# Performance work log

Hardware: AMD Instinct MI355X
Metric: run time of the kernel (lower is better)

Reference implementation:

```python
import jax, jax.numpy as jnp
import numpy as np

DEGREE = 8


def setup_inputs() -> dict:
    key = jax.random.key(0)
    k1, k2 = jax.random.split(key)
    x = jax.random.normal(k1, (8192, 1024), dtype=jnp.float32)
    # xavier_normal-ish scale for coeffs [input_dim, output_dim, degree+1]
    std = (2.0 / (1024 + 1024)) ** 0.5
    cheby_coeffs = jax.random.normal(k2, (1024, 1024, DEGREE + 1), dtype=jnp.float32) * std
    return {"x": x, "cheby_coeffs": cheby_coeffs}


def _cheby(x, degree):
    # x: [B, I] in [-1, 1]; returns T: [B, I, degree+1]
    T = [jnp.ones_like(x), x]
    for n in range(2, degree + 1):
        T.append(2.0 * x * T[-1] - T[-2])
    return jnp.stack(T, axis=-1)


def reference(x, cheby_coeffs) -> jnp.ndarray:
    input_dim = cheby_coeffs.shape[0]
    degree = cheby_coeffs.shape[-1] - 1
    x = x.reshape(-1, input_dim)
    xmin = jnp.min(x, axis=1, keepdims=True)
    xmax = jnp.max(x, axis=1, keepdims=True)
    x = 2.0 * (x - xmin) / (xmax - xmin) - 1.0
    T = _cheby(x, degree)  # [B, I, D+1]
    y = jnp.einsum('bij,ioj->bo', T, cheby_coeffs)
    return y
```

## Files before the change

### kernel.cpp

```cpp
#include <hip/hip_runtime.h>
#include <hip/hip_bf16.h>


typedef __attribute__((ext_vector_type(8))) short bf16x8s;
typedef __attribute__((ext_vector_type(4))) float f32x4;

constexpr int BROWS = 8192;
constexpr int IDIM  = 1024;
constexpr int ODIM  = 1024;
constexpr int DEG1  = 9;
constexpr int KP    = 8;
constexpr int KD    = IDIM * KP;
constexpr int KH    = KD / 2;

__device__ __forceinline__ ushort f2bf(float f) {
  return ((__hip_bfloat16_raw)__float2bfloat16(f)).x;
}

__device__ __forceinline__ void gload_lds16(const void* g, void* l) {
  __builtin_amdgcn_global_load_lds(
      (const __attribute__((address_space(1))) unsigned int*)g,
      (__attribute__((address_space(3))) unsigned int*)l, 16, 0, 0);
}

__global__ __launch_bounds__(256) void zero_bias_kernel(float* __restrict__ bias) {
  bias[blockIdx.x * 256 + threadIdx.x] = 0.0f;
}

__global__ __launch_bounds__(256) void build_a_kernel(const float* __restrict__ x,
                                                      ushort* __restrict__ A2) {
  __shared__ float red[8];
  const int b = blockIdx.x, t = threadIdx.x, lane = t & 63, wv = t >> 6;
  const float* xr = x + (size_t)b * IDIM;
  const float4 v = ((const float4*)xr)[t];
  float mn = fminf(fminf(v.x, v.y), fminf(v.z, v.w));
  float mx = fmaxf(fmaxf(v.x, v.y), fmaxf(v.z, v.w));
#pragma unroll
  for (int off = 32; off >= 1; off >>= 1) {
    mn = fminf(mn, __shfl_xor(mn, off));
    mx = fmaxf(mx, __shfl_xor(mx, off));
  }
  if (lane == 0) { red[wv] = mn; red[4 + wv] = mx; }
  __syncthreads();
  mn = fminf(fminf(red[0], red[1]), fminf(red[2], red[3]));
  mx = fmaxf(fmaxf(red[4], red[5]), fmaxf(red[6], red[7]));
  const float sc = 2.0f / (mx - mn);
  const float of = -mn * sc - 1.0f;

  uint4* adst = (uint4*)(A2 + (size_t)b * KD);
#pragma unroll
  for (int c = 0; c < 4; ++c) {
    const int i = c * 256 + t;
    const float xn = fmaf(sc, xr[i], of);
    const float T2 = 2.f * xn * xn - 1.f;
    const float T3 = 2.f * xn * T2 - xn;
    const float T4 = 2.f * xn * T3 - T2;
    const float T5 = 2.f * xn * T4 - T3;
    const float T6 = 2.f * xn * T5 - T4;
    const float T7 = 2.f * xn * T6 - T5;
    const float T8 = 2.f * xn * T7 - T6;
    uint4 w;
    w.x = (uint)f2bf(xn) | ((uint)f2bf(T2) << 16);
    w.y = (uint)f2bf(T3) | ((uint)f2bf(T4) << 16);
    w.z = (uint)f2bf(T5) | ((uint)f2bf(T6) << 16);
    w.w = (uint)f2bf(T7) | ((uint)f2bf(T8) << 16);
    adst[i] = w;
  }
}

__global__ __launch_bounds__(256) void build_b_kernel(const float* __restrict__ coeffs,
                                                      ushort* __restrict__ B2T,
                                                      float* __restrict__ bias) {
  __shared__ __align__(16) ushort tile[64 * 256];
  __shared__ float lb[64];
  const int i0 = blockIdx.x * 32;
  const int o0 = blockIdx.y * 64;
  const int t  = threadIdx.x;
  if (t < 64) lb[t] = 0.0f;
  __syncthreads();
  for (int idx = t; idx < 18432; idx += 256) {
    const int i_l = idx / 576;
    const int rem = idx - i_l * 576;
    const float v = coeffs[((size_t)(i0 + i_l) * ODIM + o0) * DEG1 + rem];
    const int o_l = rem / 9;
    const int j   = rem - o_l * 9;
    if (j == 0) atomicAdd(&lb[o_l], v);
    else tile[o_l * 256 + i_l * KP + (j - 1)] = f2bf(v);
  }
  __syncthreads();
  for (int idx = t; idx < 2048; idx += 256) {
    const int o_l = idx >> 5;
    const int w   = idx & 31;
    uint4* gdst = (uint4*)(B2T + (size_t)(o0 + o_l) * KD + i0 * KP);
    gdst[w] = ((const uint4*)tile)[idx];
  }
  if (t < 64) atomicAdd(&bias[o0 + t], lb[t]);
}

__global__ __launch_bounds__(512, 4) void gemm_kernel(const ushort* __restrict__ A2,
                                                      const ushort* __restrict__ B2T,
                                                      const float* __restrict__ bias,
                                                      float* __restrict__ out) {
  constexpr int BK = 64;
  __shared__ __align__(16) ushort Sm[32768];
  const int t    = threadIdx.x;
  const int wave = t >> 6;
  const int lane = t & 63;
  const int g    = wave >> 2;
  const int w4   = wave & 3;
  const int wr   = w4 >> 1;
  const int wc   = w4 & 1;
  const int c16  = lane & 15;
  const int quad = lane >> 4;
  const int rowBase = blockIdx.y * 128;
  const int colBase = blockIdx.x * 128;

  ushort* As = Sm + g * 8192;
  ushort* Bs = Sm + 16384 + g * 8192;

  const int tp   = t & 255;
  const int srow = tp >> 3;
  const int scol = (tp & 7) ^ (srow & 7);
  const ushort* aB = A2  + (size_t)(rowBase + srow) * KD + (size_t)g * KH + scol * 8;
  const ushort* bB = B2T + (size_t)(colBase + srow) * KD + (size_t)g * KH + scol * 8;
  ushort* lA = As + tp * 8;
  ushort* lB = Bs + tp * 8;

  f32x4 acc[4][4];
#pragma unroll
  for (int a = 0; a < 4; ++a)
#pragma unroll
    for (int b = 0; b < 4; ++b) acc[a][b] = (f32x4){0.f, 0.f, 0.f, 0.f};

  for (int ip = 0; ip < KH / BK; ++ip) {
    const size_t ko = (size_t)ip * BK;
    __syncthreads();
#pragma unroll
    for (int rr = 0; rr < 4; ++rr) {
      gload_lds16(aB + (size_t)rr * 32 * KD + ko, lA + rr * 2048);
      gload_lds16(bB + (size_t)rr * 32 * KD + ko, lB + rr * 2048);
    }
    __syncthreads();

#pragma unroll
    for (int kh = 0; kh < 2; ++kh) {
      const int cx = ((kh * 4 + quad) ^ (c16 & 7)) * 8;
      bf16x8s afr[4], bfr[4];
#pragma unroll
      for (int tm = 0; tm < 4; ++tm)
        afr[tm] = *(const bf16x8s*)&As[(wr * 64 + tm * 16 + c16) * BK + cx];
#pragma unroll
      for (int tn = 0; tn < 4; ++tn)
        bfr[tn] = *(const bf16x8s*)&Bs[(wc * 64 + tn * 16 + c16) * BK + cx];
#pragma unroll
      for (int tm = 0; tm < 4; ++tm)
#pragma unroll
        for (int tn = 0; tn < 4; ++tn)
          acc[tm][tn] = __builtin_amdgcn_mfma_f32_16x16x32_bf16(afr[tm], bfr[tn],
                                                                acc[tm][tn], 0, 0, 0);
    }
  }

  __syncthreads();
  float* Ct = (float*)Sm;
  if (g == 1) {
#pragma unroll
    for (int tm = 0; tm < 4; ++tm)
#pragma unroll
      for (int tn = 0; tn < 4; ++tn) {
        const int lr0 = wr * 64 + tm * 16 + quad * 4;
        const int cl  = wc * 64 + tn * 16 + c16;
#pragma unroll
        for (int r = 0; r < 4; ++r) Ct[(lr0 + r) * 128 + cl] = acc[tm][tn][r];
      }
  }
  __syncthreads();
  if (g == 0) {
#pragma unroll
    for (int tm = 0; tm < 4; ++tm)
#pragma unroll
      for (int tn = 0; tn < 4; ++tn) {
        const int lr0 = wr * 64 + tm * 16 + quad * 4;
        const int cl  = wc * 64 + tn * 16 + c16;
        const float bv = bias[colBase + cl];
#pragma unroll
        for (int r = 0; r < 4; ++r)
          out[(size_t)(rowBase + lr0 + r) * ODIM + colBase + cl] =
              acc[tm][tn][r] + Ct[(lr0 + r) * 128 + cl] + bv;
      }
  }
}

extern "C" void kernel_launch(void* const* d_in, const int* in_sizes, int n_in,
                              void* d_out, int out_size, void* d_ws, size_t ws_size,
                              hipStream_t stream) {
  const float* x      = (const float*)d_in[0];
  const float* coeffs = (const float*)d_in[1];
  float* out = (float*)d_out;

  char* ws = (char*)d_ws;
  float*  bias = (float*)ws;
  ushort* B2T  = (ushort*)(ws + 65536);
  ushort* A2   = (ushort*)(ws + 65536 + (size_t)ODIM * KD * 2);

  zero_bias_kernel<<<ODIM / 256, 256, 0, stream>>>(bias);
  build_a_kernel<<<BROWS, 256, 0, stream>>>(x, A2);
  build_b_kernel<<<dim3(IDIM / 32, ODIM / 64), 256, 0, stream>>>(coeffs, B2T, bias);
  gemm_kernel<<<dim3(ODIM / 128, BROWS / 128), 512, 0, stream>>>(A2, B2T, bias, out);
}
```

Measured before the change: 314.6 us.

## Restructure GEMM into triple-buffered 256x128 tiles with prefetch and block swizzle

The GEMM drops the split-K design, where two wave groups each covered half of K and were reduced through shared memory. Each block now computes a 256x128 tile over the full K using eight waves. Global-to-LDS loads are triple-buffered and issued two iterations ahead, with explicit vmcnt waits, raw barriers and setprio around the MFMA bursts. A block-index swizzle improves L2 reuse. This aims to hide load latency behind MFMA work and drop the split-K reduction, at the cost of more LDS per block and lower occupancy.

```diff
diff --git a/kernel.cpp b/kernel.cpp
--- a/kernel.cpp
+++ b/kernel.cpp
@@ -11,7 +11,6 @@
 constexpr int DEG1  = 9;
 constexpr int KP    = 8;
 constexpr int KD    = IDIM * KP;
-constexpr int KH    = KD / 2;
 
 __device__ __forceinline__ ushort f2bf(float f) {
   return ((__hip_bfloat16_raw)__float2bfloat16(f)).x;
@@ -97,97 +96,116 @@
   if (t < 64) atomicAdd(&bias[o0 + t], lb[t]);
 }
 
-__global__ __launch_bounds__(512, 4) void gemm_kernel(const ushort* __restrict__ A2,
+#define GEMM_PHASE(CX, ISSUE_STMT, TAILWAIT_STMT)                                 \
+  {                                                                               \
+    bf16x8s afr[4], bfr[4];                                                       \
+    _Pragma("unroll")                                                             \
+    for (int m = 0; m < 4; ++m)                                                   \
+      afr[m] = *(const bf16x8s*)&Asb[aoff + m * (16 * 64) + (CX)];                \
+    _Pragma("unroll")                                                             \
+    for (int n = 0; n < 4; ++n)                                                   \
+      bfr[n] = *(const bf16x8s*)&Bsb[boff + n * (16 * 64) + (CX)];                \
+    ISSUE_STMT;                                                                   \
+    __builtin_amdgcn_s_barrier();                                                 \
+    asm volatile("s_waitcnt lgkmcnt(0)" ::: "memory");                            \
+    __builtin_amdgcn_s_setprio(1);                                                \
+    _Pragma("unroll")                                                             \
+    for (int m = 0; m < 4; ++m)                                                   \
+      _Pragma("unroll")                                                           \
+      for (int n = 0; n < 4; ++n)                                                 \
+        acc[m][n] = __builtin_amdgcn_mfma_f32_16x16x32_bf16(afr[m], bfr[n],       \
+                                                            acc[m][n], 0, 0, 0);  \
+    __builtin_amdgcn_s_setprio(0);                                                \
+    TAILWAIT_STMT;                                                                \
+    __builtin_amdgcn_s_barrier();                                                 \
+  }
+
+__global__ __launch_bounds__(512, 2) void gemm_kernel(const ushort* __restrict__ A2,
                                                       const ushort* __restrict__ B2T,
                                                       const float* __restrict__ bias,
                                                       float* __restrict__ out) {
-  constexpr int BK = 64;
-  __shared__ __align__(16) ushort Sm[32768];
+  constexpr int BK    = 64;
+  constexpr int KT    = KD / BK;
+  constexpr int ABUF  = 256 * BK;
+  constexpr int BBUF  = 128 * BK;
+  constexpr int BUFSZ = ABUF + BBUF;
+  __shared__ __align__(16) ushort Sm[3 * BUFSZ];
+
   const int t    = threadIdx.x;
+  const int lane = t & 63;
   const int wave = t >> 6;
-  const int lane = t & 63;
-  const int g    = wave >> 2;
-  const int w4   = wave & 3;
-  const int wr   = w4 >> 1;
-  const int wc   = w4 & 1;
+  const int wr   = wave >> 1;
+  const int wc   = wave & 1;
   const int c16  = lane & 15;
   const int quad = lane >> 4;
-  const int rowBase = blockIdx.y * 128;
-  const int colBase = blockIdx.x * 128;
-
-  ushort* As = Sm + g * 8192;
-  ushort* Bs = Sm + 16384 + g * 8192;
-
-  const int tp   = t & 255;
-  const int srow = tp >> 3;
-  const int scol = (tp & 7) ^ (srow & 7);
-  const ushort* aB = A2  + (size_t)(rowBase + srow) * KD + (size_t)g * KH + scol * 8;
-  const ushort* bB = B2T + (size_t)(colBase + srow) * KD + (size_t)g * KH + scol * 8;
-  ushort* lA = As + tp * 8;
-  ushort* lB = Bs + tp * 8;
+
+  const int orig = blockIdx.y * 8 + blockIdx.x;
+  const int swz  = (orig & 7) * 32 + (orig >> 3);
+  const int rowBase = (swz >> 3) * 256;
+  const int colBase = (swz & 7) * 128;
+
+  const int trow = t >> 3;
+  const int scol = (t & 7) ^ (trow & 7);
+  const ushort* aB = A2  + (size_t)(rowBase + trow) * KD + scol * 8;
+  const ushort* bB = B2T + (size_t)(colBase + trow) * KD + scol * 8;
+  ushort* uA = Sm + t * 8;
+  ushort* uB = Sm + ABUF + t * 8;
+
+  auto issA = [&](int buf, size_t ko, int a) {
+    gload_lds16(aB + (size_t)a * (64 * KD) + ko, uA + buf * BUFSZ + a * 4096);
+  };
+  auto issB = [&](int buf, size_t ko, int b2) {
+    gload_lds16(bB + (size_t)b2 * (64 * KD) + ko, uB + buf * BUFSZ + b2 * 4096);
+  };
+
+  const int aoff = (wr * 64 + c16) * BK;
+  const int boff = (wc * 64 + c16) * BK;
+  const int cx0  = ((0 + quad) ^ (c16 & 7)) * 8;
+  const int cx1  = ((4 + quad) ^ (c16 & 7)) * 8;
 
   f32x4 acc[4][4];
 #pragma unroll
-  for (int a = 0; a < 4; ++a)
-#pragma unroll
-    for (int b = 0; b < 4; ++b) acc[a][b] = (f32x4){0.f, 0.f, 0.f, 0.f};
-
-  for (int ip = 0; ip < KH / BK; ++ip) {
-    const size_t ko = (size_t)ip * BK;
-    __syncthreads();
-#pragma unroll
-    for (int rr = 0; rr < 4; ++rr) {
-      gload_lds16(aB + (size_t)rr * 32 * KD + ko, lA + rr * 2048);
-      gload_lds16(bB + (size_t)rr * 32 * KD + ko, lB + rr * 2048);
+  for (int m = 0; m < 4; ++m)
+#pragma unroll
+    for (int n = 0; n < 4; ++n) acc[m][n] = (f32x4){0.f, 0.f, 0.f, 0.f};
+
+  issA(0, 0, 0); issA(0, 0, 1); issA(0, 0, 2); issA(0, 0, 3);
+  issB(0, 0, 0); issB(0, 0, 1);
+  issA(1, BK, 0); issA(1, BK, 1); issA(1, BK, 2); issA(1, BK, 3);
+  issB(1, BK, 0); issB(1, BK, 1);
+  asm volatile("s_waitcnt vmcnt(6)" ::: "memory");
+  __builtin_amdgcn_s_barrier();
+
+  int cur = 0;
+  for (int it = 0; it < KT; ++it) {
+    const ushort* Asb = Sm + cur * BUFSZ;
+    const ushort* Bsb = Asb + ABUF;
+    const int nb = (cur >= 1) ? cur - 1 : 2;
+    const size_t ko = (size_t)(it + 2) * BK;
+    const bool pf = (it < KT - 2);
+
+    GEMM_PHASE(cx0,
+      if (pf) { issA(nb, ko, 0); issA(nb, ko, 1); issA(nb, ko, 2); },
+      ;);
+    GEMM_PHASE(cx1,
+      if (pf) { issA(nb, ko, 3); issB(nb, ko, 0); issB(nb, ko, 1); },
+      if (pf)              { asm volatile("s_waitcnt vmcnt(6)" ::: "memory"); }
+      else if (it == KT-2) { asm volatile("s_waitcnt vmcnt(0)" ::: "memory"); });
+
+    cur = (cur == 2) ? 0 : cur + 1;
+  }
+
+#pragma unroll
+  for (int n = 0; n < 4; ++n) {
+    const int col = colBase + wc * 64 + n * 16 + c16;
+    const float bv = bias[col];
+#pragma unroll
+    for (int m = 0; m < 4; ++m) {
+      const int r0 = rowBase + wr * 64 + m * 16 + quad * 4;
+#pragma unroll
+      for (int r = 0; r < 4; ++r)
+        out[(size_t)(r0 + r) * ODIM + col] = acc[m][n][r] + bv;
     }
-    __syncthreads();
-
-#pragma unroll
-    for (int kh = 0; kh < 2; ++kh) {
-      const int cx = ((kh * 4 + quad) ^ (c16 & 7)) * 8;
-      bf16x8s afr[4], bfr[4];
-#pragma unroll
-      for (int tm = 0; tm < 4; ++tm)
-        afr[tm] = *(const bf16x8s*)&As[(wr * 64 + tm * 16 + c16) * BK + cx];
-#pragma unroll
-      for (int tn = 0; tn < 4; ++tn)
-        bfr[tn] = *(const bf16x8s*)&Bs[(wc * 64 + tn * 16 + c16) * BK + cx];
-#pragma unroll
-      for (int tm = 0; tm < 4; ++tm)
-#pragma unroll
-        for (int tn = 0; tn < 4; ++tn)
-          acc[tm][tn] = __builtin_amdgcn_mfma_f32_16x16x32_bf16(afr[tm], bfr[tn],
-                                                                acc[tm][tn], 0, 0, 0);
-    }
-  }
-
-  __syncthreads();
-  float* Ct = (float*)Sm;
-  if (g == 1) {
-#pragma unroll
-    for (int tm = 0; tm < 4; ++tm)
-#pragma unroll
-      for (int tn = 0; tn < 4; ++tn) {
-        const int lr0 = wr * 64 + tm * 16 + quad * 4;
-        const int cl  = wc * 64 + tn * 16 + c16;
-#pragma unroll
-        for (int r = 0; r < 4; ++r) Ct[(lr0 + r) * 128 + cl] = acc[tm][tn][r];
-      }
-  }
-  __syncthreads();
-  if (g == 0) {
-#pragma unroll
-    for (int tm = 0; tm < 4; ++tm)
-#pragma unroll
-      for (int tn = 0; tn < 4; ++tn) {
-        const int lr0 = wr * 64 + tm * 16 + quad * 4;
-        const int cl  = wc * 64 + tn * 16 + c16;
-        const float bv = bias[colBase + cl];
-#pragma unroll
-        for (int r = 0; r < 4; ++r)
-          out[(size_t)(rowBase + lr0 + r) * ODIM + colBase + cl] =
-              acc[tm][tn][r] + Ct[(lr0 + r) * 128 + cl] + bv;
-      }
   }
 }
 
@@ -206,5 +224,5 @@
   zero_bias_kernel<<<ODIM / 256, 256, 0, stream>>>(bias);
   build_a_kernel<<<BROWS, 256, 0, stream>>>(x, A2);
   build_b_kernel<<<dim3(IDIM / 32, ODIM / 64), 256, 0, stream>>>(coeffs, B2T, bias);
-  gemm_kernel<<<dim3(ODIM / 128, BROWS / 128), 512, 0, stream>>>(A2, B2T, bias, out);
-}
+  gemm_kernel<<<dim3(ODIM / 128, BROWS / 256), 512, 0, stream>>>(A2, B2T, bias, out);
+}
```

Measured after the change: 291.4 us. 7.4% less time.
